# Kernel tuning notes

Hardware: AMD Instinct MI355X
Metric: run time of the kernel (lower is better)

## Reference

```python
import jax, jax.numpy as jnp
import numpy as np

M, N, K, GROUP, BITS = 8192, 4096, 4096, 128, 4
NGROUPS = K // GROUP  # 32


def setup_inputs() -> dict:
    key = jax.random.key(0)
    k1, k2, k3, k4 = jax.random.split(key, 4)
    A = jax.random.normal(k1, (M, K), dtype=jnp.float32)
    # packed int4: each int32 entry holds one storage byte (two 4-bit nibbles), values 0..255
    qweight = jax.random.randint(k2, (N, K // 2), 0, 256, dtype=jnp.int32)
    scales = jax.random.uniform(k3, (N, NGROUPS), dtype=jnp.float32) * 0.02 + 0.001
    zeros = jax.random.randint(k4, (N, NGROUPS), 0, 16).astype(jnp.float32)
    return {"A": A, "qweight": qweight, "scales": scales, "zeros": zeros}


def dequantize(qweight, scales, zeros):
    # unpack two 4-bit nibbles per storage byte: col i of unpacked = (byte >> 4*(i%2)) & 0xF
    low = jnp.bitwise_and(qweight, 0xF)                      # [N, K//2]
    high = jnp.bitwise_and(qweight >> BITS, 0xF)             # [N, K//2]
    w = jnp.stack([low, high], axis=-1).reshape(N, K).astype(scales.dtype)  # interleaved, [N, K]
    # per-group dequant: (w - zero) * scale, group along K
    wg = w.reshape(N, NGROUPS, GROUP)
    wdq = (wg - zeros[:, :, None]) * scales[:, :, None]
    return wdq.reshape(N, K)


def reference(A, qweight, scales, zeros):
    W = dequantize(qweight, scales, zeros)  # [N, K]
    return jnp.einsum("mk,nk->mn", A, W)    # [M, N]
```

## Files before the change

kernel.cpp:

```cpp
#include <hip/hip_runtime.h>
#include <hip/hip_bf16.h>

typedef __bf16 bf16x8 __attribute__((ext_vector_type(8)));
typedef float  f32x4  __attribute__((ext_vector_type(4)));
typedef __attribute__((address_space(3))) char* lds3_t;

#define M_DIM 8192
#define N_DIM 4096
#define K_DIM 4096
#define NG    32
#define KHALF (K_DIM / 2)

__global__ __launch_bounds__(256) void cvtA_kernel(const float* __restrict__ A,
                                                   __bf16* __restrict__ Ab,
                                                   long n8) {
    long i = (long)blockIdx.x * blockDim.x + threadIdx.x;
    long stride = (long)gridDim.x * blockDim.x;
    const float4* A4 = (const float4*)A;
    for (long p = i; p < n8; p += stride) {
        float4 v0 = A4[2 * p];
        float4 v1 = A4[2 * p + 1];
        bf16x8 o;
        o[0] = (__bf16)v0.x; o[1] = (__bf16)v0.y;
        o[2] = (__bf16)v0.z; o[3] = (__bf16)v0.w;
        o[4] = (__bf16)v1.x; o[5] = (__bf16)v1.y;
        o[6] = (__bf16)v1.z; o[7] = (__bf16)v1.w;
        *(bf16x8*)(Ab + p * 8) = o;
    }
}

__global__ __launch_bounds__(256) void deqW_kernel(const int* __restrict__ qw,
                                                   const float* __restrict__ sc,
                                                   const float* __restrict__ zr,
                                                   __bf16* __restrict__ Wb) {
    long i = (long)blockIdx.x * blockDim.x + threadIdx.x;
    long stride = (long)gridDim.x * blockDim.x;
    const long nch = (long)N_DIM * (KHALF / 4);
    const int4* q4 = (const int4*)qw;
    for (long p = i; p < nch; p += stride) {
        int n  = (int)(p >> 9);
        int cj = (int)(p & 511);
        int i0 = cj * 4;
        int g  = i0 >> 6;
        float s = sc[n * NG + g];
        float z = zr[n * NG + g];
        int4 qv = q4[p];
        bf16x8 o;
        int b;
        b = qv.x; o[0] = (__bf16)(((float)(b & 0xF) - z) * s);
                  o[1] = (__bf16)(((float)((b >> 4) & 0xF) - z) * s);
        b = qv.y; o[2] = (__bf16)(((float)(b & 0xF) - z) * s);
                  o[3] = (__bf16)(((float)((b >> 4) & 0xF) - z) * s);
        b = qv.z; o[4] = (__bf16)(((float)(b & 0xF) - z) * s);
                  o[5] = (__bf16)(((float)((b >> 4) & 0xF) - z) * s);
        b = qv.w; o[6] = (__bf16)(((float)(b & 0xF) - z) * s);
                  o[7] = (__bf16)(((float)((b >> 4) & 0xF) - z) * s);
        *(bf16x8*)(Wb + (long)n * K_DIM + i0 * 2) = o;
    }
}

#define BM 256
#define BN 256
#define BK 64
#define NT (K_DIM / BK)

#define SB0 __builtin_amdgcn_sched_barrier(0)
#define BAR do { SB0; __builtin_amdgcn_s_barrier(); } while (0)
#define LGKM(N) do { asm volatile("s_waitcnt lgkmcnt(" #N ")" ::: "memory"); SB0; } while (0)
#define VMW(N)  do { asm volatile("s_waitcnt vmcnt(" #N ")"  ::: "memory"); SB0; } while (0)
#define PRIO1 __builtin_amdgcn_s_setprio(1)
#define PRIO0 __builtin_amdgcn_s_setprio(0)

#define DSR(dst, base, OFFS) \
    asm volatile("ds_read_b128 %0, %1 offset:" OFFS : "=v"(dst) : "v"(base))

#define RD_A(BASEV, Q, K, O0, O1, O2, O3)          \
  do {                                             \
    DSR(a##Q##k##K[0], BASEV, O0);                 \
    DSR(a##Q##k##K[1], BASEV, O1);                 \
    DSR(a##Q##k##K[2], BASEV, O2);                 \
    DSR(a##Q##k##K[3], BASEV, O3);                 \
  } while (0)

#define RD_B(BASEV, Q, K, O0, O1)                  \
  do {                                             \
    DSR(b##Q##k##K[0], BASEV, O0);                 \
    DSR(b##Q##k##K[1], BASEV, O1);                 \
  } while (0)

#define ACC1(QM, MM, QN, NN, KK)                                                 \
  acc[(QM) * 4 + (MM)][(QN) * 2 + (NN)] = __builtin_amdgcn_mfma_f32_16x16x32_bf16( \
      a##QM##k##KK[MM], b##QN##k##KK[NN], acc[(QM) * 4 + (MM)][(QN) * 2 + (NN)], 0, 0, 0)

#define MFMA8(QM, QN, KK)       \
  do {                          \
    PRIO1;                      \
    ACC1(QM, 0, QN, 0, KK);     \
    ACC1(QM, 0, QN, 1, KK);     \
    ACC1(QM, 1, QN, 0, KK);     \
    ACC1(QM, 1, QN, 1, KK);     \
    ACC1(QM, 2, QN, 0, KK);     \
    ACC1(QM, 2, QN, 1, KK);     \
    ACC1(QM, 3, QN, 0, KK);     \
    ACC1(QM, 3, QN, 1, KK);     \
    PRIO0;                      \
  } while (0)

#define STAGE(SRC, MATOFF, H, DB, KT)                                                              \
  do {                                                                                             \
    __builtin_amdgcn_global_load_lds(                                                              \
        (__attribute__((address_space(1))) void*)((SRC) + (long)((H) * 128) * (K_DIM * 2) +        \
                                                  (long)(KT) * (BK * 2)),                          \
        (__attribute__((address_space(3))) void*)(lds + (DB) + (MATOFF) + (H) * 16384 + ldst),     \
        16, 0, 0);                                                                                 \
    __builtin_amdgcn_global_load_lds(                                                              \
        (__attribute__((address_space(1))) void*)((SRC) + (long)((H) * 128 + 64) * (K_DIM * 2) +   \
                                                  (long)(KT) * (BK * 2)),                          \
        (__attribute__((address_space(3))) void*)(lds + (DB) + (MATOFF) + (H) * 16384 + 8192 +     \
                                                  ldst),                                           \
        16, 0, 0);                                                                                 \
  } while (0)

#define TILE(P, PN, JJ)                                                           \
  do {                                                                            \
    const int jp1 = (JJ) + 1, jp2 = (JJ) + 2;                                     \
                                                     \
    BAR;                                                                          \
                                    \
    RD_B(ba##P##0, 1, 0, "4096", "6144");                                         \
    if (jp1 < NT) STAGE(Bsrc, 32768, 0, (PN) * 65536, jp1);                       \
    LGKM(6);                                                                      \
    MFMA8(0, 0, 0);                                                               \
                   \
    if (jp1 < NT) STAGE(Bsrc, 32768, 1, (PN) * 65536, jp1);                       \
    LGKM(2);                                                                      \
    MFMA8(1, 0, 0);                                                               \
                                                      \
    BAR;                                                                          \
                       \
    RD_A(aa##P##1, 0, 1, "0", "2048", "4096", "6144");                            \
    RD_B(ba##P##1, 1, 1, "4096", "6144");                                         \
    LGKM(6);                                                                      \
    MFMA8(1, 1, 0);                                                               \
            \
    RD_A(aa##P##1, 1, 1, "8192", "10240", "12288", "14336");                      \
    MFMA8(0, 1, 0);                                                               \
                                                      \
    BAR;                                                                          \
                         \
    RD_B(ba##P##1, 0, 1, "0", "2048");                                            \
    LGKM(6);                                                                      \
    MFMA8(0, 1, 1);                                                               \
            \
    LGKM(2);                                                                      \
    MFMA8(1, 1, 1);                                                               \
    VMW(0);                                                                       \
                                                      \
    BAR;                                                                          \
                                              \
    if (jp1 < NT) {                                                               \
      RD_A(aa##PN##0, 0, 0, "0", "2048", "4096", "6144");                         \
      RD_B(ba##PN##0, 0, 0, "0", "2048");                                         \
    }                                                                             \
    if (jp2 < NT) STAGE(Asrc, 0, 0, (P) * 65536, jp2);                            \
    LGKM(6);                                                                      \
    MFMA8(1, 0, 1);                                                               \
           \
    if (jp1 < NT) RD_A(aa##PN##0, 1, 0, "8192", "10240", "12288", "14336");       \
    if (jp2 < NT) STAGE(Asrc, 0, 1, (P) * 65536, jp2);                            \
    MFMA8(0, 0, 1);                                                               \
  } while (0)

__global__ __launch_bounds__(512, 2) void gemm8p(const __bf16* __restrict__ A,
                                                 const __bf16* __restrict__ B,
                                                 float* __restrict__ C) {
    __shared__ __attribute__((aligned(128))) char lds[131072];

    const int nwg = (M_DIM / BM) * (N_DIM / BN);
    int bid = blockIdx.x;
    int sw  = (bid & 7) * (nwg >> 3) + (bid >> 3);
    int mt = sw >> 4, ntl = sw & 15;
    int bm0 = mt * BM, bn0 = ntl * BN;

    int tid  = threadIdx.x;
    int lane = tid & 63;
    int wid  = tid >> 6;
    int wr   = wid >> 2;
    int wc   = wid & 3;

    f32x4 acc[8][4];
    f32x4 vz = {0.f, 0.f, 0.f, 0.f};
#pragma unroll
    for (int m = 0; m < 8; ++m)
#pragma unroll
        for (int n = 0; n < 4; ++n) acc[m][n] = vz;

    bf16x8 a0k0[4], a1k0[4], a0k1[4], a1k1[4];
    bf16x8 b0k0[2], b1k0[2], b0k1[2], b1k1[2];

    int srow  = tid >> 3;
    int scolb = ((tid & 7) ^ (srow & 7)) * 16;
    const char* Asrc = (const char*)(A + (long)(bm0 + srow) * K_DIM) + scolb;
    const char* Bsrc = (const char*)(B + (long)(bn0 + srow) * K_DIM) + scolb;
    int ldst = tid * 16;

    int lrow = lane & 15;
    int rc0  = (((lane >> 4) ^ (lane & 7)) << 4);
    int rc1  = rc0 ^ 64;
    int aoff = wr * 16384 + lrow * 128;
    int boff = 32768 + (wc >> 1) * 16384 + ((wc & 1) * 64 + lrow) * 128;

    lds3_t aa00 = (lds3_t)(lds + aoff + rc0);
    lds3_t aa01 = (lds3_t)(lds + aoff + rc1);
    lds3_t aa10 = (lds3_t)(lds + 65536 + aoff + rc0);
    lds3_t aa11 = (lds3_t)(lds + 65536 + aoff + rc1);
    lds3_t ba00 = (lds3_t)(lds + boff + rc0);
    lds3_t ba01 = (lds3_t)(lds + boff + rc1);
    lds3_t ba10 = (lds3_t)(lds + 65536 + boff + rc0);
    lds3_t ba11 = (lds3_t)(lds + 65536 + boff + rc1);

    STAGE(Asrc, 0,     0, 0, 0);
    STAGE(Asrc, 0,     1, 0, 0);
    STAGE(Bsrc, 32768, 0, 0, 0);
    STAGE(Bsrc, 32768, 1, 0, 0);
    STAGE(Asrc, 0,     0, 65536, 1);
    STAGE(Asrc, 0,     1, 65536, 1);
    VMW(2);
    BAR;
    RD_A(aa00, 0, 0, "0", "2048", "4096", "6144");
    RD_B(ba00, 0, 0, "0", "2048");
    RD_A(aa00, 1, 0, "8192", "10240", "12288", "14336");

    for (int j = 0; j < NT; j += 2) {
        TILE(0, 1, j);
        TILE(1, 0, j + 1);
    }

    int crow0 = bm0 + wr * 128 + (lane >> 4) * 4;
    int ccol0 = bn0 + wc * 64 + (lane & 15);
#pragma unroll
    for (int m = 0; m < 8; ++m)
#pragma unroll
        for (int n = 0; n < 4; ++n) {
            long base = (long)(crow0 + m * 16) * N_DIM + (ccol0 + n * 16);
#pragma unroll
            for (int jj = 0; jj < 4; ++jj)
                C[base + (long)jj * N_DIM] = acc[m][n][jj];
        }
}

__global__ __launch_bounds__(256) void gemm_fallback(const float* __restrict__ A,
                                                     const int* __restrict__ qw,
                                                     const float* __restrict__ sc,
                                                     const float* __restrict__ zr,
                                                     float* __restrict__ C) {
    __shared__ float Ash[16][17];
    __shared__ float Wsh[16][17];
    int tx = threadIdx.x & 15, ty = threadIdx.x >> 4;
    int m = blockIdx.y * 16 + ty;
    int n = blockIdx.x * 16 + tx;
    float s = 0.f;
    for (int k0 = 0; k0 < K_DIM; k0 += 16) {
        Ash[ty][tx] = A[(long)m * K_DIM + k0 + tx];
        {
            int nn = blockIdx.x * 16 + ty;
            int kk = k0 + tx;
            int q = qw[(long)nn * KHALF + (kk >> 1)];
            int nib = (kk & 1) ? ((q >> 4) & 0xF) : (q & 0xF);
            int g = kk >> 7;
            Wsh[ty][tx] = ((float)nib - zr[nn * NG + g]) * sc[nn * NG + g];
        }
        __syncthreads();
#pragma unroll
        for (int kk = 0; kk < 16; ++kk)
            s += Ash[ty][kk] * Wsh[tx][kk];
        __syncthreads();
    }
    C[(long)m * N_DIM + n] = s;
}

extern "C" void kernel_launch(void* const* d_in, const int* in_sizes, int n_in,
                              void* d_out, int out_size, void* d_ws, size_t ws_size,
                              hipStream_t stream) {
    const float* A  = (const float*)d_in[0];
    const int*   qw = (const int*)d_in[1];
    const float* sc = (const float*)d_in[2];
    const float* zr = (const float*)d_in[3];
    float* C = (float*)d_out;

    const size_t needA = (size_t)M_DIM * K_DIM * 2;
    const size_t needW = (size_t)N_DIM * K_DIM * 2;

    if (ws_size >= needA + needW) {
        __bf16* Ab = (__bf16*)d_ws;
        __bf16* Wb = (__bf16*)((char*)d_ws + needA);
        cvtA_kernel<<<2048, 256, 0, stream>>>(A, Ab, (long)M_DIM * K_DIM / 8);
        deqW_kernel<<<2048, 256, 0, stream>>>(qw, sc, zr, Wb);
        gemm8p<<<(M_DIM / BM) * (N_DIM / BN), 512, 0, stream>>>(Ab, Wb, C);
    } else {
        dim3 g(N_DIM / 16, M_DIM / 16);
        gemm_fallback<<<g, 256, 0, stream>>>(A, qw, sc, zr, C);
    }
}
```

Measured before the change: 271.7 us.

## Fuse fp32-to-bf16 conversion of A into GEMM main loop via register staging

Drops the separate cvtA kernel. The GEMM now loads fp32 A tiles straight from global memory into registers two K-tiles ahead, packs them to bf16 and writes them into swizzled LDS with ds_write_b128. This interleaves with the existing B global_load_lds pipeline and adjusts vmcnt waits. It removes the 64MB bf16 A round trip and one kernel launch. In exchange, every N-tile block re-reads fp32 A, which is twice the bytes, and the kernel takes on extra VGPR pressure and VALU conversion work in the hot loop.

```diff
diff --git a/kernel.cpp b/kernel.cpp
--- a/kernel.cpp
+++ b/kernel.cpp
@@ -10,24 +10,6 @@
 #define K_DIM 4096
 #define NG    32
 #define KHALF (K_DIM / 2)
-
-__global__ __launch_bounds__(256) void cvtA_kernel(const float* __restrict__ A,
-                                                   __bf16* __restrict__ Ab,
-                                                   long n8) {
-    long i = (long)blockIdx.x * blockDim.x + threadIdx.x;
-    long stride = (long)gridDim.x * blockDim.x;
-    const float4* A4 = (const float4*)A;
-    for (long p = i; p < n8; p += stride) {
-        float4 v0 = A4[2 * p];
-        float4 v1 = A4[2 * p + 1];
-        bf16x8 o;
-        o[0] = (__bf16)v0.x; o[1] = (__bf16)v0.y;
-        o[2] = (__bf16)v0.z; o[3] = (__bf16)v0.w;
-        o[4] = (__bf16)v1.x; o[5] = (__bf16)v1.y;
-        o[6] = (__bf16)v1.z; o[7] = (__bf16)v1.w;
-        *(bf16x8*)(Ab + p * 8) = o;
-    }
-}
 
 __global__ __launch_bounds__(256) void deqW_kernel(const int* __restrict__ qw,
                                                    const float* __restrict__ sc,
@@ -73,6 +55,8 @@
 
 #define DSR(dst, base, OFFS) \
     asm volatile("ds_read_b128 %0, %1 offset:" OFFS : "=v"(dst) : "v"(base))
+#define DSW(addr, val, OFFS) \
+    asm volatile("ds_write_b128 %0, %1 offset:" OFFS :: "v"(addr), "v"(val))
 
 #define RD_A(BASEV, Q, K, O0, O1, O2, O3)          \
   do {                                             \
@@ -121,57 +105,80 @@
         16, 0, 0);                                                                                 \
   } while (0)
 
-#define TILE(P, PN, JJ)                                                           \
+#define LOADAF(KT)                       \
+  do {                                   \
+    af0 = pA0[(KT) * 16 + 0];            \
+    af1 = pA0[(KT) * 16 + 1];            \
+    af2 = pA0[(KT) * 16 + 2];            \
+    af3 = pA0[(KT) * 16 + 3];            \
+    af4 = pA1[(KT) * 16 + 0];            \
+    af5 = pA1[(KT) * 16 + 1];            \
+    af6 = pA1[(KT) * 16 + 2];            \
+    af7 = pA1[(KT) * 16 + 3];            \
+  } while (0)
+
+#define PACK(DSTV, PLO, PHI)                                       \
+  do {                                                             \
+    DSTV[0] = (__bf16)(PLO).x; DSTV[1] = (__bf16)(PLO).y;          \
+    DSTV[2] = (__bf16)(PLO).z; DSTV[3] = (__bf16)(PLO).w;          \
+    DSTV[4] = (__bf16)(PHI).x; DSTV[5] = (__bf16)(PHI).y;          \
+    DSTV[6] = (__bf16)(PHI).z; DSTV[7] = (__bf16)(PHI).w;          \
+  } while (0)
+
+#define TILE(P, PN, JJ, WV, TW)                                                   \
   do {                                                                            \
     const int jp1 = (JJ) + 1, jp2 = (JJ) + 2;                                     \
-                                                     \
     BAR;                                                                          \
-                                    \
+                               \
     RD_B(ba##P##0, 1, 0, "4096", "6144");                                         \
     if (jp1 < NT) STAGE(Bsrc, 32768, 0, (PN) * 65536, jp1);                       \
-    LGKM(6);                                                                      \
+    LGKM(6); TW                                                                   \
     MFMA8(0, 0, 0);                                                               \
-                   \
+                                          \
     if (jp1 < NT) STAGE(Bsrc, 32768, 1, (PN) * 65536, jp1);                       \
-    LGKM(2);                                                                      \
+    LGKM(2); TW                                                                   \
     MFMA8(1, 0, 0);                                                               \
-                                                      \
     BAR;                                                                          \
-                       \
+                        \
+    if (jp2 < NT) LOADAF(jp2);                                                    \
     RD_A(aa##P##1, 0, 1, "0", "2048", "4096", "6144");                            \
     RD_B(ba##P##1, 1, 1, "4096", "6144");                                         \
-    LGKM(6);                                                                      \
+    LGKM(6); TW                                                                   \
     MFMA8(1, 1, 0);                                                               \
-            \
+                                                \
     RD_A(aa##P##1, 1, 1, "8192", "10240", "12288", "14336");                      \
     MFMA8(0, 1, 0);                                                               \
-                                                      \
     BAR;                                                                          \
-                         \
+                                                \
     RD_B(ba##P##1, 0, 1, "0", "2048");                                            \
-    LGKM(6);                                                                      \
+    LGKM(6); TW                                                                   \
     MFMA8(0, 1, 1);                                                               \
             \
-    LGKM(2);                                                                      \
+    LGKM(2); TW                                                                   \
     MFMA8(1, 1, 1);                                                               \
-    VMW(0);                                                                       \
-                                                      \
+    WV                                                                            \
     BAR;                                                                          \
-                                              \
+                 \
+    if (jp2 < NT) {                                                               \
+      PACK(oa, af0, af1); PACK(ob, af2, af3);                                     \
+      DSW(awa##P, oa, "0"); DSW(awb##P, ob, "0");                                 \
+    }                                                                             \
     if (jp1 < NT) {                                                               \
       RD_A(aa##PN##0, 0, 0, "0", "2048", "4096", "6144");                         \
       RD_B(ba##PN##0, 0, 0, "0", "2048");                                         \
     }                                                                             \
-    if (jp2 < NT) STAGE(Asrc, 0, 0, (P) * 65536, jp2);                            \
-    LGKM(6);                                                                      \
+    LGKM(6); TW                                                                   \
     MFMA8(1, 0, 1);                                                               \
-           \
+                      \
+    if (jp2 < NT) {                                                               \
+      PACK(oa, af4, af5); PACK(ob, af6, af7);                                     \
+      DSW(awa##P, oa, "16384"); DSW(awb##P, ob, "16384");                         \
+    }                                                                             \
     if (jp1 < NT) RD_A(aa##PN##0, 1, 0, "8192", "10240", "12288", "14336");       \
-    if (jp2 < NT) STAGE(Asrc, 0, 1, (P) * 65536, jp2);                            \
     MFMA8(0, 0, 1);                                                               \
   } while (0)
 
-__global__ __launch_bounds__(512, 2) void gemm8p(const __bf16* __restrict__ A,
+__global__ __launch_bounds__(512, 2) void gemm8p(const float* __restrict__ Af,
                                                  const __bf16* __restrict__ B,
                                                  float* __restrict__ C) {
     __shared__ __attribute__((aligned(128))) char lds[131072];
@@ -197,12 +204,23 @@
 
     bf16x8 a0k0[4], a1k0[4], a0k1[4], a1k1[4];
     bf16x8 b0k0[2], b1k0[2], b0k1[2], b1k1[2];
+    float4 af0, af1, af2, af3, af4, af5, af6, af7;
+    bf16x8 oa, ob;
 
     int srow  = tid >> 3;
     int scolb = ((tid & 7) ^ (srow & 7)) * 16;
-    const char* Asrc = (const char*)(A + (long)(bm0 + srow) * K_DIM) + scolb;
     const char* Bsrc = (const char*)(B + (long)(bn0 + srow) * K_DIM) + scolb;
     int ldst = tid * 16;
+
+    int wrow = tid >> 2;
+    int ws0  = (tid & 3) * 2;
+    int sw0  = (ws0 ^ (wrow & 7)) * 16;
+    lds3_t awa0 = (lds3_t)(lds + wrow * 128 + sw0);
+    lds3_t awb0 = (lds3_t)(lds + wrow * 128 + (sw0 ^ 16));
+    lds3_t awa1 = awa0 + 65536;
+    lds3_t awb1 = awb0 + 65536;
+    const float4* pA0 = (const float4*)(Af + (long)(bm0 + wrow) * K_DIM) + ws0 * 2;
+    const float4* pA1 = pA0 + (long)32 * K_DIM;
 
     int lrow = lane & 15;
     int rc0  = (((lane >> 4) ^ (lane & 7)) << 4);
@@ -219,22 +237,31 @@
     lds3_t ba10 = (lds3_t)(lds + 65536 + boff + rc0);
     lds3_t ba11 = (lds3_t)(lds + 65536 + boff + rc1);
 
-    STAGE(Asrc, 0,     0, 0, 0);
-    STAGE(Asrc, 0,     1, 0, 0);
     STAGE(Bsrc, 32768, 0, 0, 0);
     STAGE(Bsrc, 32768, 1, 0, 0);
-    STAGE(Asrc, 0,     0, 65536, 1);
-    STAGE(Asrc, 0,     1, 65536, 1);
-    VMW(2);
+    LOADAF(0);
+    PACK(oa, af0, af1); PACK(ob, af2, af3);
+    DSW(awa0, oa, "0");     DSW(awb0, ob, "0");
+    PACK(oa, af4, af5); PACK(ob, af6, af7);
+    DSW(awa0, oa, "16384"); DSW(awb0, ob, "16384");
+    LOADAF(1);
+    PACK(oa, af0, af1); PACK(ob, af2, af3);
+    DSW(awa1, oa, "0");     DSW(awb1, ob, "0");
+    PACK(oa, af4, af5); PACK(ob, af6, af7);
+    DSW(awa1, oa, "16384"); DSW(awb1, ob, "16384");
+    LGKM(0);
+    VMW(0);
     BAR;
     RD_A(aa00, 0, 0, "0", "2048", "4096", "6144");
     RD_B(ba00, 0, 0, "0", "2048");
     RD_A(aa00, 1, 0, "8192", "10240", "12288", "14336");
 
-    for (int j = 0; j < NT; j += 2) {
-        TILE(0, 1, j);
-        TILE(1, 0, j + 1);
+    for (int j = 0; j < NT - 2; j += 2) {
+        TILE(0, 1, j, VMW(8);, );
+        TILE(1, 0, j + 1, VMW(8);, );
     }
+    TILE(0, 1, NT - 2, VMW(0);, );
+    TILE(1, 0, NT - 1, VMW(0);, LGKM(0););
 
     int crow0 = bm0 + wr * 128 + (lane >> 4) * 4;
     int ccol0 = bn0 + wc * 64 + (lane & 15);
@@ -288,15 +315,12 @@
     const float* zr = (const float*)d_in[3];
     float* C = (float*)d_out;
 
-    const size_t needA = (size_t)M_DIM * K_DIM * 2;
     const size_t needW = (size_t)N_DIM * K_DIM * 2;
 
-    if (ws_size >= needA + needW) {
-        __bf16* Ab = (__bf16*)d_ws;
-        __bf16* Wb = (__bf16*)((char*)d_ws + needA);
-        cvtA_kernel<<<2048, 256, 0, stream>>>(A, Ab, (long)M_DIM * K_DIM / 8);
+    if (ws_size >= needW) {
+        __bf16* Wb = (__bf16*)d_ws;
         deqW_kernel<<<2048, 256, 0, stream>>>(qw, sc, zr, Wb);
-        gemm8p<<<(M_DIM / BM) * (N_DIM / BN), 512, 0, stream>>>(Ab, Wb, C);
+        gemm8p<<<(M_DIM / BM) * (N_DIM / BN), 512, 0, stream>>>(A, Wb, C);
     } else {
         dim3 g(N_DIM / 16, M_DIM / 16);
         gemm_fallback<<<g, 256, 0, stream>>>(A, qw, sc, zr, C);
```

Measured after the change: 470.2 us. 1.73x slower.

## Load B operand directly from global into registers instead of via LDS

Applied to the files above, without the earlier changes.

The B (dequantized weight) tile is no longer staged through LDS. Each wave loads its own B fragments straight from global memory with global_load_dwordx4, and LDS shrinks to 64KB holding only double-buffered A. This removes B's LDS writes and reads and two of the per-tile barriers. In exchange it relies on global/L2 latency being hidden by the waitcnt schedule, and B rows are re-fetched by the two wave rows that share them, adding global traffic.

```diff
diff --git a/kernel.cpp b/kernel.cpp
--- a/kernel.cpp
+++ b/kernel.cpp
@@ -73,6 +73,8 @@
 
 #define DSR(dst, base, OFFS) \
     asm volatile("ds_read_b128 %0, %1 offset:" OFFS : "=v"(dst) : "v"(base))
+#define GLB(dst, ptr, OFFS) \
+    asm volatile("global_load_dwordx4 %0, %1, off offset:" OFFS : "=v"(dst) : "v"(ptr))
 
 #define RD_A(BASEV, Q, K, O0, O1, O2, O3)          \
   do {                                             \
@@ -82,10 +84,10 @@
     DSR(a##Q##k##K[3], BASEV, O3);                 \
   } while (0)
 
-#define RD_B(BASEV, Q, K, O0, O1)                  \
+#define GLB_B(QN, KK, OFFS)                        \
   do {                                             \
-    DSR(b##Q##k##K[0], BASEV, O0);                 \
-    DSR(b##Q##k##K[1], BASEV, O1);                 \
+    GLB(b##QN##k##KK[0], pB##QN##0, OFFS);         \
+    GLB(b##QN##k##KK[1], pB##QN##1, OFFS);         \
   } while (0)
 
 #define ACC1(QM, MM, QN, NN, KK)                                                 \
@@ -106,75 +108,70 @@
     PRIO0;                      \
   } while (0)
 
-#define STAGE(SRC, MATOFF, H, DB, KT)                                                              \
+#define STAGE(SRC, H, DB, KT)                                                                      \
   do {                                                                                             \
     __builtin_amdgcn_global_load_lds(                                                              \
         (__attribute__((address_space(1))) void*)((SRC) + (long)((H) * 128) * (K_DIM * 2) +        \
                                                   (long)(KT) * (BK * 2)),                          \
-        (__attribute__((address_space(3))) void*)(lds + (DB) + (MATOFF) + (H) * 16384 + ldst),     \
+        (__attribute__((address_space(3))) void*)(lds + (DB) + (H) * 16384 + ldst),                \
         16, 0, 0);                                                                                 \
     __builtin_amdgcn_global_load_lds(                                                              \
         (__attribute__((address_space(1))) void*)((SRC) + (long)((H) * 128 + 64) * (K_DIM * 2) +   \
                                                   (long)(KT) * (BK * 2)),                          \
-        (__attribute__((address_space(3))) void*)(lds + (DB) + (MATOFF) + (H) * 16384 + 8192 +     \
-                                                  ldst),                                           \
+        (__attribute__((address_space(3))) void*)(lds + (DB) + (H) * 16384 + 8192 + ldst),         \
         16, 0, 0);                                                                                 \
   } while (0)
 
-#define TILE(P, PN, JJ)                                                           \
+#define TILE(P, PN, JJ, W1, W7)                                                   \
   do {                                                                            \
     const int jp1 = (JJ) + 1, jp2 = (JJ) + 2;                                     \
-                                                     \
+            \
+    GLB_B(1, 0, "0");                                                             \
+    W1                                                                            \
+    LGKM(4);                                                                      \
+    MFMA8(0, 0, 0);                                                               \
+                                                   \
+    LGKM(0);                                                                      \
+    MFMA8(1, 0, 0);                                                               \
+          \
+    RD_A(aa##P##1, 0, 1, "0", "2048", "4096", "6144");                            \
+    GLB_B(1, 1, "64");                                                            \
+    VMW(2);                                                                       \
+    MFMA8(1, 1, 0);                                                               \
+                             \
+    RD_A(aa##P##1, 1, 1, "8192", "10240", "12288", "14336");                      \
+    LGKM(4);                                                                      \
+    MFMA8(0, 1, 0);                                                               \
+                             \
+    GLB_B(0, 1, "64");                                                            \
+    VMW(2);                                                                       \
+    MFMA8(0, 1, 1);                                                               \
+                                      \
+    LGKM(0);                                                                      \
+    MFMA8(1, 1, 1);                                                               \
+          \
     BAR;                                                                          \
-                                    \
-    RD_B(ba##P##0, 1, 0, "4096", "6144");                                         \
-    if (jp1 < NT) STAGE(Bsrc, 32768, 0, (PN) * 65536, jp1);                       \
-    LGKM(6);                                                                      \
-    MFMA8(0, 0, 0);                                                               \
-                   \
-    if (jp1 < NT) STAGE(Bsrc, 32768, 1, (PN) * 65536, jp1);                       \
-    LGKM(2);                                                                      \
-    MFMA8(1, 0, 0);                                                               \
-                                                      \
-    BAR;                                                                          \
-                       \
-    RD_A(aa##P##1, 0, 1, "0", "2048", "4096", "6144");                            \
-    RD_B(ba##P##1, 1, 1, "4096", "6144");                                         \
-    LGKM(6);                                                                      \
-    MFMA8(1, 1, 0);                                                               \
-            \
-    RD_A(aa##P##1, 1, 1, "8192", "10240", "12288", "14336");                      \
-    MFMA8(0, 1, 0);                                                               \
-                                                      \
-    BAR;                                                                          \
-                         \
-    RD_B(ba##P##1, 0, 1, "0", "2048");                                            \
-    LGKM(6);                                                                      \
-    MFMA8(0, 1, 1);                                                               \
-            \
-    LGKM(2);                                                                      \
-    MFMA8(1, 1, 1);                                                               \
-    VMW(0);                                                                       \
-                                                      \
-    BAR;                                                                          \
-                                              \
+                                                \
     if (jp1 < NT) {                                                               \
+      GLB_B(0, 0, "128");                                                         \
       RD_A(aa##PN##0, 0, 0, "0", "2048", "4096", "6144");                         \
-      RD_B(ba##PN##0, 0, 0, "0", "2048");                                         \
+      RD_A(aa##PN##0, 1, 0, "8192", "10240", "12288", "14336");                   \
     }                                                                             \
-    if (jp2 < NT) STAGE(Asrc, 0, 0, (P) * 65536, jp2);                            \
-    LGKM(6);                                                                      \
+    if (jp2 < NT) {                                                               \
+      STAGE(Asrc, 0, (P) * 32768, jp2);                                           \
+      STAGE(Asrc, 1, (P) * 32768, jp2);                                           \
+    }                                                                             \
+    W7                                                                            \
     MFMA8(1, 0, 1);                                                               \
-           \
-    if (jp1 < NT) RD_A(aa##PN##0, 1, 0, "8192", "10240", "12288", "14336");       \
-    if (jp2 < NT) STAGE(Asrc, 0, 1, (P) * 65536, jp2);                            \
+                            \
+    pB00 += 128; pB01 += 128; pB10 += 128; pB11 += 128;                           \
     MFMA8(0, 0, 1);                                                               \
   } while (0)
 
 __global__ __launch_bounds__(512, 2) void gemm8p(const __bf16* __restrict__ A,
                                                  const __bf16* __restrict__ B,
                                                  float* __restrict__ C) {
-    __shared__ __attribute__((aligned(128))) char lds[131072];
+    __shared__ __attribute__((aligned(128))) char lds[65536];
 
     const int nwg = (M_DIM / BM) * (N_DIM / BN);
     int bid = blockIdx.x;
@@ -201,40 +198,38 @@
     int srow  = tid >> 3;
     int scolb = ((tid & 7) ^ (srow & 7)) * 16;
     const char* Asrc = (const char*)(A + (long)(bm0 + srow) * K_DIM) + scolb;
-    const char* Bsrc = (const char*)(B + (long)(bn0 + srow) * K_DIM) + scolb;
     int ldst = tid * 16;
 
     int lrow = lane & 15;
     int rc0  = (((lane >> 4) ^ (lane & 7)) << 4);
     int rc1  = rc0 ^ 64;
     int aoff = wr * 16384 + lrow * 128;
-    int boff = 32768 + (wc >> 1) * 16384 + ((wc & 1) * 64 + lrow) * 128;
-
     lds3_t aa00 = (lds3_t)(lds + aoff + rc0);
     lds3_t aa01 = (lds3_t)(lds + aoff + rc1);
-    lds3_t aa10 = (lds3_t)(lds + 65536 + aoff + rc0);
-    lds3_t aa11 = (lds3_t)(lds + 65536 + aoff + rc1);
-    lds3_t ba00 = (lds3_t)(lds + boff + rc0);
-    lds3_t ba01 = (lds3_t)(lds + boff + rc1);
-    lds3_t ba10 = (lds3_t)(lds + 65536 + boff + rc0);
-    lds3_t ba11 = (lds3_t)(lds + 65536 + boff + rc1);
-
-    STAGE(Asrc, 0,     0, 0, 0);
-    STAGE(Asrc, 0,     1, 0, 0);
-    STAGE(Bsrc, 32768, 0, 0, 0);
-    STAGE(Bsrc, 32768, 1, 0, 0);
-    STAGE(Asrc, 0,     0, 65536, 1);
-    STAGE(Asrc, 0,     1, 65536, 1);
-    VMW(2);
+    lds3_t aa10 = (lds3_t)(lds + 32768 + aoff + rc0);
+    lds3_t aa11 = (lds3_t)(lds + 32768 + aoff + rc1);
+
+    const char* pB00 = (const char*)(B + (long)(bn0 + wc * 64 +  0 + lrow) * K_DIM + ((lane >> 4) * 8));
+    const char* pB01 = (const char*)(B + (long)(bn0 + wc * 64 + 16 + lrow) * K_DIM + ((lane >> 4) * 8));
+    const char* pB10 = (const char*)(B + (long)(bn0 + wc * 64 + 32 + lrow) * K_DIM + ((lane >> 4) * 8));
+    const char* pB11 = (const char*)(B + (long)(bn0 + wc * 64 + 48 + lrow) * K_DIM + ((lane >> 4) * 8));
+
+    STAGE(Asrc, 0, 0, 0);
+    STAGE(Asrc, 1, 0, 0);
+    GLB_B(0, 0, "0");
+    STAGE(Asrc, 0, 32768, 1);
+    STAGE(Asrc, 1, 32768, 1);
+    VMW(6);
     BAR;
     RD_A(aa00, 0, 0, "0", "2048", "4096", "6144");
-    RD_B(ba00, 0, 0, "0", "2048");
     RD_A(aa00, 1, 0, "8192", "10240", "12288", "14336");
 
-    for (int j = 0; j < NT; j += 2) {
-        TILE(0, 1, j);
-        TILE(1, 0, j + 1);
-    }
+    for (int j = 0; j < NT - 2; j += 2) {
+        TILE(0, 1, j, VMW(6);, VMW(6););
+        TILE(1, 0, j + 1, VMW(6);, VMW(6););
+    }
+    TILE(0, 1, NT - 2, VMW(6);, VMW(2););
+    TILE(1, 0, NT - 1, VMW(2);, VMW(0););
 
     int crow0 = bm0 + wr * 128 + (lane >> 4) * 4;
     int ccol0 = bn0 + wc * 64 + (lane & 15);
```

Result: slower. 355.9 us (+31.0%).
